# Optimization experiments

Measured on AMD Instinct MI355X. Metric: run time of the kernel, lower is better.

## Reference

```python
import jax, jax.numpy as jnp
import numpy as np


def log_g(x):
    # log of g(x) = where(x>=0, x+0.5, sigmoid(x))
    return jnp.where(x >= 0, jnp.log(jnp.maximum(x, 0.0) + 0.5), -jax.nn.softplus(-x))


def setup_inputs() -> dict:
    key = jax.random.key(0)
    k1, k2 = jax.random.split(key)
    B, S, D = 8, 8192, 512
    x = jax.random.normal(k1, (B, S, D), dtype=jnp.float32)
    # to_hidden_and_gate weight: [2*D, D] (orthogonal init in torch; gaussian ok for reference)
    W = jax.random.normal(k2, (2 * D, D), dtype=jnp.float32) / np.sqrt(D)
    return {"x": x, "W": W}


def reference(x, W):
    # x: [B, S, D], W: [2D, D]
    hg = jnp.einsum('bsd,ed->bse', x, W)  # [B, S, 2D]
    D = x.shape[-1]
    hidden, gate = hg[..., :D], hg[..., D:]

    # log-domain minGRU (Heinsen associative scan)
    log_coeffs = -jax.nn.softplus(gate)            # log(1 - z)
    log_z = -jax.nn.softplus(-gate)                # log(z)
    log_values = log_z + log_g(hidden)             # log(z * g(h~))

    a_star = jnp.cumsum(log_coeffs, axis=1)
    log_h = a_star + jax.lax.cumlogsumexp(log_values - a_star, axis=1)
    out = jnp.exp(log_h)                           # [B, S, D]

    next_prev_hidden = out[:, -1:]
    return out, next_prev_hidden
```

## Files before the change

### kernel.cpp

```cpp
#include <hip/hip_runtime.h>
#include <hip/hip_bf16.h>
#include <stdint.h>

typedef float f32x4 __attribute__((ext_vector_type(4)));
typedef __bf16 bf16x8 __attribute__((ext_vector_type(8)));
typedef unsigned short ushort8 __attribute__((ext_vector_type(8)));

#define NB 8
#define NS 8192
#define ND 512
#define NM (NB * NS)
#define NK 512

__device__ __forceinline__ unsigned short f2bf(float f) {
  unsigned u = __float_as_uint(f);
  u += 0x7FFFu + ((u >> 16) & 1u);
  return (unsigned short)(u >> 16);
}

__device__ __forceinline__ uint32_t cvtpk(float lo, float hi) {
  uint32_t r;
  asm("v_cvt_pk_bf16_f32 %0, %1, %2" : "=v"(r) : "v"(lo), "v"(hi));
  return r;
}

__global__ __launch_bounds__(256) void cvt_bf16(const float* __restrict__ src,
                                                unsigned short* __restrict__ dst,
                                                int n8) {
  int i = blockIdx.x * 256 + threadIdx.x;
  if (i >= n8) return;
  const float4* s = reinterpret_cast<const float4*>(src + (size_t)i * 8);
  float4 v0 = s[0], v1 = s[1];
  ushort8 o;
  o[0] = f2bf(v0.x); o[1] = f2bf(v0.y); o[2] = f2bf(v0.z); o[3] = f2bf(v0.w);
  o[4] = f2bf(v1.x); o[5] = f2bf(v1.y); o[6] = f2bf(v1.z); o[7] = f2bf(v1.w);
  *reinterpret_cast<ushort8*>(dst + (size_t)i * 8) = o;
}

__global__ __launch_bounds__(256) void gemm_ab(const float* __restrict__ x,
                                               const unsigned short* __restrict__ wb,
                                               uint32_t* __restrict__ pk,
                                               float* __restrict__ aggA,
                                               float* __restrict__ aggB) {
  __shared__ __align__(16) char lds[2 * 24576];
  __shared__ float aggL[128];

  const int tid = threadIdx.x;
  const int w = tid >> 6;
  const int lane = tid & 63;
  const int wr = w >> 1;
  const int wc = w & 1;
  const int orig = blockIdx.x;
  const int wg = (orig & 7) * 512 + (orig >> 3);
  const int mblk = wg >> 3;
  const int nblk = wg & 7;
  const int m0 = mblk * 128;
  const int n0 = nblk * 64;

  const int aSrc = (((lane & 7) ^ (lane >> 3)) << 2);
  const float* pAf[4];
#pragma unroll
  for (int g = 0; g < 4; ++g) {
    int row = g * 32 + w * 8 + (lane >> 3);
    pAf[g] = x + (size_t)(m0 + row) * NK + aSrc;
  }
  const int bSrc = (((lane & 3) ^ ((lane >> 2) & 3)) << 3);
  const unsigned short* pBf[2];
#pragma unroll
  for (int g = 0; g < 2; ++g) {
    int row = g * 64 + w * 16 + (lane >> 2);
    int e = (row < 64) ? (n0 + row) : (448 + n0 + row);
    pBf[g] = wb + (size_t)e * NK + bSrc;
  }

  auto stage = [&](int buf, int kt) {
    char* base = lds + buf * 24576;
    const int ko = kt << 5;
#pragma unroll
    for (int g = 0; g < 4; ++g)
      __builtin_amdgcn_global_load_lds(
          (const __attribute__((address_space(1))) void*)(pAf[g] + ko),
          (__attribute__((address_space(3))) void*)(base + (g * 4 + w) * 1024),
          16, 0, 0);
#pragma unroll
    for (int g = 0; g < 2; ++g)
      __builtin_amdgcn_global_load_lds(
          (const __attribute__((address_space(1))) void*)(pBf[g] + ko),
          (__attribute__((address_space(3))) void*)(base + 16384 + (g * 4 + w) * 1024),
          16, 0, 0);
  };

  f32x4 acc[4][4];
#pragma unroll
  for (int i = 0; i < 4; ++i)
#pragma unroll
    for (int j = 0; j < 4; ++j) acc[i][j] = (f32x4)0.0f;

  const int fr = lane & 15;
  const int kg = lane >> 4;

  stage(0, 0);
  __syncthreads();

#pragma unroll 1
  for (int kt = 0; kt < 16; ++kt) {
    const int cur = kt & 1;
    if (kt < 15) stage(cur ^ 1, kt + 1);

    const char* ldsA = lds + cur * 24576;
    const char* ldsB = ldsA + 16384;
    bf16x8 af[4], bfr[4];
#pragma unroll
    for (int i = 0; i < 4; ++i) {
      int rowA = wr * 64 + i * 16 + fr;
      int s0 = ((2 * kg) ^ (fr & 7)) << 4;
      int s1 = ((2 * kg + 1) ^ (fr & 7)) << 4;
      f32x4 q0 = *reinterpret_cast<const f32x4*>(ldsA + rowA * 128 + s0);
      f32x4 q1 = *reinterpret_cast<const f32x4*>(ldsA + rowA * 128 + s1);
      uint4 u;
      u.x = cvtpk(q0[0], q0[1]);
      u.y = cvtpk(q0[2], q0[3]);
      u.z = cvtpk(q1[0], q1[1]);
      u.w = cvtpk(q1[2], q1[3]);
      af[i] = *reinterpret_cast<bf16x8*>(&u);
      int rowB = ((i < 2) ? (wc * 32 + i * 16) : (64 + wc * 32 + (i - 2) * 16)) + fr;
      bfr[i] = *reinterpret_cast<const bf16x8*>(ldsB + rowB * 64 + ((kg ^ (fr & 3)) << 4));
    }
#pragma unroll
    for (int i = 0; i < 4; ++i)
#pragma unroll
      for (int j = 0; j < 4; ++j)
        acc[i][j] = __builtin_amdgcn_mfma_f32_16x16x32_bf16(af[i], bfr[j], acc[i][j], 0, 0, 0);

    __syncthreads();
  }

  const float LOG2E = 1.44269504f;
  float A64[2], B64[2];
#pragma unroll
  for (int n = 0; n < 2; ++n) {
    const int ch = wc * 32 + n * 16 + fr;
    float Am[4], Bm[4];
#pragma unroll
    for (int m = 0; m < 4; ++m) {
      float As = 1.0f, Bs = 0.0f;
#pragma unroll
      for (int r = 0; r < 4; ++r) {
        float hid = acc[m][n][r];
        float gat = acc[m][n + 2][r];
        float ex1 = __builtin_amdgcn_exp2f(gat * LOG2E);
        float a = __builtin_amdgcn_rcpf(1.0f + ex1);
        float z = 1.0f - a;
        float ex2 = __builtin_amdgcn_exp2f(-hid * LOG2E);
        float gn = __builtin_amdgcn_rcpf(1.0f + ex2);
        float g = (hid >= 0.0f) ? (hid + 0.5f) : gn;
        float bb = z * g;
        int row = 64 * wr + 16 * m + 4 * kg + r;
        pk[(size_t)(m0 + row) * ND + n0 + ch] =
            ((uint32_t)f2bf(bb) << 16) | (uint32_t)f2bf(a);
        Bs = fmaf(a, Bs, bb);
        As *= a;
      }
      Am[m] = As; Bm[m] = Bs;
    }
#pragma unroll
    for (int m = 0; m < 4; ++m) {
      float pA_ = __shfl_xor(Am[m], 16);
      float pB_ = __shfl_xor(Bm[m], 16);
      Bm[m] = (kg & 1) ? fmaf(Am[m], pB_, Bm[m]) : fmaf(pA_, Bm[m], pB_);
      Am[m] *= pA_;
      pA_ = __shfl_xor(Am[m], 32);
      pB_ = __shfl_xor(Bm[m], 32);
      Bm[m] = (kg & 2) ? fmaf(Am[m], pB_, Bm[m]) : fmaf(pA_, Bm[m], pB_);
      Am[m] *= pA_;
    }
    float As = Am[0], Bs = Bm[0];
#pragma unroll
    for (int m = 1; m < 4; ++m) { Bs = fmaf(Am[m], Bs, Bm[m]); As *= Am[m]; }
    A64[n] = As; B64[n] = Bs;
  }
  if (wr == 0 && kg == 0) {
#pragma unroll
    for (int n = 0; n < 2; ++n) {
      int ch = wc * 32 + n * 16 + fr;
      aggL[ch * 2] = A64[n];
      aggL[ch * 2 + 1] = B64[n];
    }
  }
  __syncthreads();
  if (wr == 1 && kg == 0) {
#pragma unroll
    for (int n = 0; n < 2; ++n) {
      int ch = wc * 32 + n * 16 + fr;
      float A0 = aggL[ch * 2], B0 = aggL[ch * 2 + 1];
      size_t o = (size_t)mblk * ND + n0 + ch;
      aggA[o] = A0 * A64[n];
      aggB[o] = fmaf(A64[n], B0, B64[n]);
    }
  }
}

__global__ __launch_bounds__(256) void scan_pass2(const uint32_t* __restrict__ pk,
                                                  const float* __restrict__ aggA,
                                                  const float* __restrict__ aggB,
                                                  float* __restrict__ out,
                                                  float* __restrict__ nextp) {
  int bid = blockIdx.x;
  int b = bid >> 6;
  int c = bid & 63;
  int d2 = threadIdx.x;

  float h0 = 0.0f, h1 = 0.0f;
  for (int cc = 0; cc < c; ++cc) {
    int o = (b * 64 + cc) * ND + d2 * 2;
    float2 Aa = *reinterpret_cast<const float2*>(&aggA[o]);
    float2 Bb = *reinterpret_cast<const float2*>(&aggB[o]);
    h0 = fmaf(Aa.x, h0, Bb.x);
    h1 = fmaf(Aa.y, h1, Bb.y);
  }
  size_t base = (size_t)(b * NS + c * 128) * ND + d2 * 2;
#pragma unroll 4
  for (int t = 0; t < 128; ++t) {
    size_t idx = base + (size_t)t * ND;
    uint2 v = *reinterpret_cast<const uint2*>(pk + idx);
    float a0 = __uint_as_float(v.x << 16);
    float b0 = __uint_as_float(v.x & 0xffff0000u);
    float a1 = __uint_as_float(v.y << 16);
    float b1 = __uint_as_float(v.y & 0xffff0000u);
    h0 = fmaf(a0, h0, b0);
    h1 = fmaf(a1, h1, b1);
    *reinterpret_cast<float2*>(&out[idx]) = make_float2(h0, h1);
  }
  if (c == 63) {
    *reinterpret_cast<float2*>(&nextp[b * ND + d2 * 2]) = make_float2(h0, h1);
  }
}

extern "C" void kernel_launch(void* const* d_in, const int* in_sizes, int n_in,
                              void* d_out, int out_size, void* d_ws, size_t ws_size,
                              hipStream_t stream) {
  const float* x = (const float*)d_in[0];
  const float* W = (const float*)d_in[1];
  float* out = (float*)d_out;

  char* ws = (char*)d_ws;
  uint32_t* pk = (uint32_t*)ws;
  unsigned short* wbf = (unsigned short*)(ws + (size_t)128 * 1024 * 1024);
  float* aggA = (float*)(ws + (size_t)129 * 1024 * 1024);
  float* aggB = (float*)(ws + (size_t)130 * 1024 * 1024);
  float* nextp = out + (size_t)NM * ND;

  cvt_bf16<<<256, 256, 0, stream>>>(W, wbf, (1024 * NK) / 8);
  gemm_ab<<<4096, 256, 0, stream>>>(x, wbf, pk, aggA, aggB);
  scan_pass2<<<512, 256, 0, stream>>>(pk, aggA, aggB, out, nextp);
}
```

Before: 230.5 us.

## Load GEMM operands directly from global into registers, bypassing LDS

Replaces the LDS double-buffered staging (global_load_lds plus swizzled LDS reads and per-iteration barriers) with direct per-lane global loads into register double buffers, and sets launch bounds to two blocks per CU. The aim is to remove LDS traffic and __syncthreads stalls from the K loop. In exchange, each wave loads its own A and B fragments, so data shared across waves is fetched redundantly from global memory or cache. The register buffers also raise register pressure, which the occupancy hint must accommodate.

```diff
diff --git a/kernel.cpp b/kernel.cpp
--- a/kernel.cpp
+++ b/kernel.cpp
@@ -37,12 +37,11 @@
   *reinterpret_cast<ushort8*>(dst + (size_t)i * 8) = o;
 }
 
-__global__ __launch_bounds__(256) void gemm_ab(const float* __restrict__ x,
-                                               const unsigned short* __restrict__ wb,
-                                               uint32_t* __restrict__ pk,
-                                               float* __restrict__ aggA,
-                                               float* __restrict__ aggB) {
-  __shared__ __align__(16) char lds[2 * 24576];
+__global__ __launch_bounds__(256, 2) void gemm_ab(const float* __restrict__ x,
+                                                  const unsigned short* __restrict__ wb,
+                                                  uint32_t* __restrict__ pk,
+                                                  float* __restrict__ aggA,
+                                                  float* __restrict__ aggB) {
   __shared__ float aggL[128];
 
   const int tid = threadIdx.x;
@@ -57,83 +56,81 @@
   const int m0 = mblk * 128;
   const int n0 = nblk * 64;
 
-  const int aSrc = (((lane & 7) ^ (lane >> 3)) << 2);
-  const float* pAf[4];
-#pragma unroll
-  for (int g = 0; g < 4; ++g) {
-    int row = g * 32 + w * 8 + (lane >> 3);
-    pAf[g] = x + (size_t)(m0 + row) * NK + aSrc;
-  }
-  const int bSrc = (((lane & 3) ^ ((lane >> 2) & 3)) << 3);
-  const unsigned short* pBf[2];
-#pragma unroll
-  for (int g = 0; g < 2; ++g) {
-    int row = g * 64 + w * 16 + (lane >> 2);
-    int e = (row < 64) ? (n0 + row) : (448 + n0 + row);
-    pBf[g] = wb + (size_t)e * NK + bSrc;
-  }
-
-  auto stage = [&](int buf, int kt) {
-    char* base = lds + buf * 24576;
-    const int ko = kt << 5;
-#pragma unroll
-    for (int g = 0; g < 4; ++g)
-      __builtin_amdgcn_global_load_lds(
-          (const __attribute__((address_space(1))) void*)(pAf[g] + ko),
-          (__attribute__((address_space(3))) void*)(base + (g * 4 + w) * 1024),
-          16, 0, 0);
-#pragma unroll
-    for (int g = 0; g < 2; ++g)
-      __builtin_amdgcn_global_load_lds(
-          (const __attribute__((address_space(1))) void*)(pBf[g] + ko),
-          (__attribute__((address_space(3))) void*)(base + 16384 + (g * 4 + w) * 1024),
-          16, 0, 0);
-  };
-
-  f32x4 acc[4][4];
-#pragma unroll
-  for (int i = 0; i < 4; ++i)
-#pragma unroll
-    for (int j = 0; j < 4; ++j) acc[i][j] = (f32x4)0.0f;
-
   const int fr = lane & 15;
   const int kg = lane >> 4;
 
-  stage(0, 0);
-  __syncthreads();
-
+  const float* pAd[4];
+#pragma unroll
+  for (int i = 0; i < 4; ++i)
+    pAd[i] = x + (size_t)(m0 + wr * 64 + i * 16 + fr) * NK + kg * 8;
+  const unsigned short* pBd[4];
+#pragma unroll
+  for (int i = 0; i < 4; ++i) {
+    int rowB = ((i < 2) ? (wc * 32 + i * 16) : (64 + wc * 32 + (i - 2) * 16)) + fr;
+    int e = (rowB < 64) ? (n0 + rowB) : (448 + n0 + rowB);
+    pBd[i] = wb + (size_t)e * NK + kg * 8;
+  }
+
+  f32x4 acc[4][4];
+#pragma unroll
+  for (int i = 0; i < 4; ++i)
+#pragma unroll
+    for (int j = 0; j < 4; ++j) acc[i][j] = (f32x4)0.0f;
+
+  f32x4 A0r[8], A1r[8];
+  uint4 B0r[4], B1r[4];
+
+#define LOADA(DST, KT)                                                        \
+  {                                                                           \
+    _Pragma("unroll")                                                         \
+    for (int i = 0; i < 4; ++i) {                                             \
+      DST[2 * i]     = *reinterpret_cast<const f32x4*>(pAd[i] + (KT) * 32);   \
+      DST[2 * i + 1] = *reinterpret_cast<const f32x4*>(pAd[i] + (KT) * 32 + 4); \
+    }                                                                         \
+  }
+#define LOADB(DST, KT)                                                        \
+  {                                                                           \
+    _Pragma("unroll")                                                         \
+    for (int i = 0; i < 4; ++i)                                               \
+      DST[i] = *reinterpret_cast<const uint4*>(pBd[i] + (KT) * 32);           \
+  }
+#define COMPUTE(AR, BR)                                                       \
+  {                                                                           \
+    bf16x8 af[4], bfr[4];                                                     \
+    _Pragma("unroll")                                                         \
+    for (int i = 0; i < 4; ++i) {                                             \
+      uint4 u;                                                                \
+      u.x = cvtpk(AR[2 * i][0], AR[2 * i][1]);                                \
+      u.y = cvtpk(AR[2 * i][2], AR[2 * i][3]);                                \
+      u.z = cvtpk(AR[2 * i + 1][0], AR[2 * i + 1][1]);                        \
+      u.w = cvtpk(AR[2 * i + 1][2], AR[2 * i + 1][3]);                        \
+      af[i] = *reinterpret_cast<bf16x8*>(&u);                                 \
+      bfr[i] = *reinterpret_cast<bf16x8*>(&BR[i]);                            \
+    }                                                                         \
+    _Pragma("unroll")                                                         \
+    for (int i = 0; i < 4; ++i)                                               \
+      _Pragma("unroll")                                                       \
+      for (int j = 0; j < 4; ++j)                                             \
+        acc[i][j] = __builtin_amdgcn_mfma_f32_16x16x32_bf16(af[i], bfr[j],    \
+                                                            acc[i][j], 0, 0, 0); \
+  }
+
+  LOADA(A0r, 0);
+  LOADB(B0r, 0);
 #pragma unroll 1
-  for (int kt = 0; kt < 16; ++kt) {
-    const int cur = kt & 1;
-    if (kt < 15) stage(cur ^ 1, kt + 1);
-
-    const char* ldsA = lds + cur * 24576;
-    const char* ldsB = ldsA + 16384;
-    bf16x8 af[4], bfr[4];
-#pragma unroll
-    for (int i = 0; i < 4; ++i) {
-      int rowA = wr * 64 + i * 16 + fr;
-      int s0 = ((2 * kg) ^ (fr & 7)) << 4;
-      int s1 = ((2 * kg + 1) ^ (fr & 7)) << 4;
-      f32x4 q0 = *reinterpret_cast<const f32x4*>(ldsA + rowA * 128 + s0);
-      f32x4 q1 = *reinterpret_cast<const f32x4*>(ldsA + rowA * 128 + s1);
-      uint4 u;
-      u.x = cvtpk(q0[0], q0[1]);
-      u.y = cvtpk(q0[2], q0[3]);
-      u.z = cvtpk(q1[0], q1[1]);
-      u.w = cvtpk(q1[2], q1[3]);
-      af[i] = *reinterpret_cast<bf16x8*>(&u);
-      int rowB = ((i < 2) ? (wc * 32 + i * 16) : (64 + wc * 32 + (i - 2) * 16)) + fr;
-      bfr[i] = *reinterpret_cast<const bf16x8*>(ldsB + rowB * 64 + ((kg ^ (fr & 3)) << 4));
-    }
-#pragma unroll
-    for (int i = 0; i < 4; ++i)
-#pragma unroll
-      for (int j = 0; j < 4; ++j)
-        acc[i][j] = __builtin_amdgcn_mfma_f32_16x16x32_bf16(af[i], bfr[j], acc[i][j], 0, 0, 0);
-
-    __syncthreads();
-  }
+  for (int ktp = 0; ktp < 16; ktp += 2) {
+    LOADA(A1r, ktp + 1);
+    LOADB(B1r, ktp + 1);
+    COMPUTE(A0r, B0r);
+    if (ktp < 14) {
+      LOADA(A0r, ktp + 2);
+      LOADB(B0r, ktp + 2);
+    }
+    COMPUTE(A1r, B1r);
+  }
+#undef LOADA
+#undef LOADB
+#undef COMPUTE
 
   const float LOG2E = 1.44269504f;
   float A64[2], B64[2];
```

Measured after the change: 419.1 us. +81.8%, slower.
